# Kernel tuning notes

Hardware: AMD Instinct MI355X
Metric: run time of the kernel (lower is better)

Reference implementation:

```python
import jax, jax.numpy as jnp
import numpy as np

RADIUS = 1
WIN = 2 * RADIUS + 1


def setup_inputs() -> dict:
    key = jax.random.key(0)
    k1, k2 = jax.random.split(key)
    shape = (2, 64, 80, 80, 80)  # (b, c, d, h, w)
    x = jax.random.normal(k1, shape, dtype=jnp.float32)
    y = jax.random.normal(k2, shape, dtype=jnp.float32)
    return {"x": x, "y": y}


def reference(x, y):
    b, c, d, h, w = x.shape
    # zero-pad y by RADIUS on all three spatial dims
    y_padded = jnp.pad(
        y, ((0, 0), (0, 0), (RADIUS, RADIUS), (RADIUS, RADIUS), (RADIUS, RADIUS))
    )
    corrs = []
    for dz in range(WIN):
        for dy in range(WIN):
            for dx in range(WIN):
                y_win = y_padded[:, :, dz:dz + d, dy:dy + h, dx:dx + w]
                # channel-summed correlation for this offset -> [b, d, h, w]
                corrs.append(jnp.sum(x * y_win, axis=1))
    corr = jnp.stack(corrs, axis=1)
    return corr * (c ** -0.5)
```

## Files before the change

### kernel.cpp

```cpp
#include <hip/hip_runtime.h>

#define NT 320
#define TZ 4
#define TH 4
#define PZ 6
#define PH 6
#define STR 88
#define PROWS (PZ*PH)
#define NSLOT (PROWS*20)

__global__ __launch_bounds__(NT)
void wincorr_kernel(const float* __restrict__ x, const float* __restrict__ y,
                    float* __restrict__ out)
{
    __shared__ __align__(16) float buf[2][PROWS * STR];

    const long long plane = 512000;
    const int tid = threadIdx.x;
    const int twi = tid % 20;
    const int th  = (tid / 20) % TH;
    const int tz  = tid / 80;

    const int zt = blockIdx.x, ht = blockIdx.y, b = blockIdx.z;
    const int z0 = zt * TZ, h0 = ht * TH;
    const int gz = z0 + tz, gh = h0 + th, wb = 4 * twi;

    const float* xb = x + (long long)b * 64 * plane;
    const float* yb = y + (long long)b * 64 * plane;
    const long long xoff = (long long)gz * 6400 + gh * 80 + wb;

    int  goff[3], loff[3];
    bool val[3];
    const bool inr2 = (tid + 2 * NT) < NSLOT;
#pragma unroll
    for (int k = 0; k < 3; ++k) {
        int s   = tid + k * NT;
        int row = s / 20, col = s % 20;
        int pz = row / PH, py = row % PH;
        int yz = z0 - 1 + pz, yh = h0 - 1 + py;
        bool ok = (s < NSLOT) && ((unsigned)yz < 80u) && ((unsigned)yh < 80u);
        val[k]  = ok;
        goff[k] = yz * 6400 + yh * 80 + 4 * col;
        loff[k] = row * STR + 4 + 4 * col;
    }

    if (tid < 2 * PROWS) {
        int r = tid >> 1;
        int cix = (tid & 1) ? 84 : 3;
        buf[0][r * STR + cix] = 0.f;
        buf[1][r * STR + cix] = 0.f;
    }

    float4 acc[27];
#pragma unroll
    for (int o = 0; o < 27; ++o) acc[o] = make_float4(0.f, 0.f, 0.f, 0.f);

    const float4 zero4 = make_float4(0.f, 0.f, 0.f, 0.f);
    float4 v0, v1, v2;

    {
        const float* yc = yb;
        v0 = val[0] ? *(const float4*)(yc + goff[0]) : zero4;
        v1 = val[1] ? *(const float4*)(yc + goff[1]) : zero4;
        v2 = val[2] ? *(const float4*)(yc + goff[2]) : zero4;
        *(float4*)(&buf[0][loff[0]]) = v0;
        *(float4*)(&buf[0][loff[1]]) = v1;
        if (inr2) *(float4*)(&buf[0][loff[2]]) = v2;
    }
    __syncthreads();

    for (int c = 0; c < 64; ++c) {
        const float4 xv = *(const float4*)(xb + (long long)c * plane + xoff);

        if (c < 63) {
            const float* yc = yb + (long long)(c + 1) * plane;
            v0 = val[0] ? *(const float4*)(yc + goff[0]) : zero4;
            v1 = val[1] ? *(const float4*)(yc + goff[1]) : zero4;
            v2 = val[2] ? *(const float4*)(yc + goff[2]) : zero4;
        }

        const float* B = buf[c & 1];
#pragma unroll
        for (int dz = 0; dz < 3; ++dz) {
#pragma unroll
            for (int dy = 0; dy < 3; ++dy) {
                const float* rowp = B + ((tz + dz) * PH + (th + dy)) * STR + wb;
                const float4 r  = *(const float4*)(rowp + 4);
                const float rm1 = rowp[3];
                const float rp4 = rowp[8];
                const int o = (dz * 3 + dy) * 3;
                acc[o].x   += xv.x * rm1; acc[o].y   += xv.y * r.x;
                acc[o].z   += xv.z * r.y; acc[o].w   += xv.w * r.z;
                acc[o+1].x += xv.x * r.x; acc[o+1].y += xv.y * r.y;
                acc[o+1].z += xv.z * r.z; acc[o+1].w += xv.w * r.w;
                acc[o+2].x += xv.x * r.y; acc[o+2].y += xv.y * r.z;
                acc[o+2].z += xv.z * r.w; acc[o+2].w += xv.w * rp4;
            }
        }

        if (c < 63) {
            float* W = (float*)buf[(c + 1) & 1];
            *(float4*)(W + loff[0]) = v0;
            *(float4*)(W + loff[1]) = v1;
            if (inr2) *(float4*)(W + loff[2]) = v2;
        }
        __syncthreads();
    }

    float* ob = out + (long long)b * 27 * plane + xoff;
#pragma unroll
    for (int o = 0; o < 27; ++o) {
        float4 v = acc[o];
        v.x *= 0.125f; v.y *= 0.125f; v.z *= 0.125f; v.w *= 0.125f;
        *(float4*)(ob + (long long)o * plane) = v;
    }
}

extern "C" void kernel_launch(void* const* d_in, const int* in_sizes, int n_in,
                              void* d_out, int out_size, void* d_ws, size_t ws_size,
                              hipStream_t stream) {
    const float* x = (const float*)d_in[0];
    const float* y = (const float*)d_in[1];
    float* out = (float*)d_out;

    dim3 grid(80 / TZ, 80 / TH, 2);
    dim3 block(NT);
    wincorr_kernel<<<grid, block, 0, stream>>>(x, y, out);
}
```

Before: 750.6 us.

## Move the dx shift from shared-memory y reads onto x and output indexing

Instead of reading two extra unaligned scalars from shared memory per (dz,dy) row to form the dx=-1 and dx=+1 windows, each thread now reads only one aligned float4 of y. It loads two neighbouring x scalars from global memory per channel and writes the shifted results to output positions offset by one, zeroing the boundary columns explicitly. This cuts LDS reads in the inner loop and drops the padded halo columns, so the LDS row stride shrinks. In exchange it adds two scalar global loads per channel and turns the output stores into unaligned, partly scalar writes.

```diff
diff --git a/kernel.cpp b/kernel.cpp
--- a/kernel.cpp
+++ b/kernel.cpp
@@ -5,9 +5,13 @@
 #define TH 4
 #define PZ 6
 #define PH 6
-#define STR 88
+#define STR 84
 #define PROWS (PZ*PH)
 #define NSLOT (PROWS*20)
+
+__device__ __forceinline__ void store_f4u(float* p, float4 v) {
+    __builtin_memcpy(p, &v, 16);
+}
 
 __global__ __launch_bounds__(NT)
 void wincorr_kernel(const float* __restrict__ x, const float* __restrict__ y,
@@ -28,6 +32,8 @@
     const float* xb = x + (long long)b * 64 * plane;
     const float* yb = y + (long long)b * 64 * plane;
     const long long xoff = (long long)gz * 6400 + gh * 80 + wb;
+    const long long xoffm = xoff - (wb > 0 ? 1 : 0);
+    const long long xoffp = xoff + (wb < 76 ? 4 : 3);
 
     int  goff[3], loff[3];
     bool val[3];
@@ -41,14 +47,7 @@
         bool ok = (s < NSLOT) && ((unsigned)yz < 80u) && ((unsigned)yh < 80u);
         val[k]  = ok;
         goff[k] = yz * 6400 + yh * 80 + 4 * col;
-        loff[k] = row * STR + 4 + 4 * col;
-    }
-
-    if (tid < 2 * PROWS) {
-        int r = tid >> 1;
-        int cix = (tid & 1) ? 84 : 3;
-        buf[0][r * STR + cix] = 0.f;
-        buf[1][r * STR + cix] = 0.f;
+        loff[k] = row * STR + 4 * col;
     }
 
     float4 acc[27];
@@ -70,7 +69,10 @@
     __syncthreads();
 
     for (int c = 0; c < 64; ++c) {
-        const float4 xv = *(const float4*)(xb + (long long)c * plane + xoff);
+        const float* xcp = xb + (long long)c * plane;
+        const float4 xv  = *(const float4*)(xcp + xoff);
+        const float  xml = xcp[xoffm];
+        const float  xpr = xcp[xoffp];
 
         if (c < 63) {
             const float* yc = yb + (long long)(c + 1) * plane;
@@ -84,17 +86,14 @@
         for (int dz = 0; dz < 3; ++dz) {
 #pragma unroll
             for (int dy = 0; dy < 3; ++dy) {
-                const float* rowp = B + ((tz + dz) * PH + (th + dy)) * STR + wb;
-                const float4 r  = *(const float4*)(rowp + 4);
-                const float rm1 = rowp[3];
-                const float rp4 = rowp[8];
+                const float4 r = *(const float4*)(B + ((tz + dz) * PH + (th + dy)) * STR + wb);
                 const int o = (dz * 3 + dy) * 3;
-                acc[o].x   += xv.x * rm1; acc[o].y   += xv.y * r.x;
-                acc[o].z   += xv.z * r.y; acc[o].w   += xv.w * r.z;
+                acc[o].x   += xv.y * r.x; acc[o].y   += xv.z * r.y;
+                acc[o].z   += xv.w * r.z; acc[o].w   += xpr  * r.w;
                 acc[o+1].x += xv.x * r.x; acc[o+1].y += xv.y * r.y;
                 acc[o+1].z += xv.z * r.z; acc[o+1].w += xv.w * r.w;
-                acc[o+2].x += xv.x * r.y; acc[o+2].y += xv.y * r.z;
-                acc[o+2].z += xv.z * r.w; acc[o+2].w += xv.w * rp4;
+                acc[o+2].x += xml  * r.x; acc[o+2].y += xv.x * r.y;
+                acc[o+2].z += xv.y * r.z; acc[o+2].w += xv.z * r.w;
             }
         }
 
@@ -109,10 +108,25 @@
 
     float* ob = out + (long long)b * 27 * plane + xoff;
 #pragma unroll
-    for (int o = 0; o < 27; ++o) {
-        float4 v = acc[o];
-        v.x *= 0.125f; v.y *= 0.125f; v.z *= 0.125f; v.w *= 0.125f;
-        *(float4*)(ob + (long long)o * plane) = v;
+    for (int dz = 0; dz < 3; ++dz) {
+#pragma unroll
+        for (int dy = 0; dy < 3; ++dy) {
+            const int o = (dz * 3 + dy) * 3;
+            float4 a0 = acc[o], a1 = acc[o+1], a2 = acc[o+2];
+            a0.x *= 0.125f; a0.y *= 0.125f; a0.z *= 0.125f; a0.w *= 0.125f;
+            a1.x *= 0.125f; a1.y *= 0.125f; a1.z *= 0.125f; a1.w *= 0.125f;
+            a2.x *= 0.125f; a2.y *= 0.125f; a2.z *= 0.125f; a2.w *= 0.125f;
+            float* p0 = ob + (long long)(o    ) * plane;
+            float* p1 = ob + (long long)(o + 1) * plane;
+            float* p2 = ob + (long long)(o + 2) * plane;
+            if (twi < 19) store_f4u(p0 + 1, a0);
+            else { p0[1] = a0.x; p0[2] = a0.y; p0[3] = a0.z; }
+            if (twi == 0) p0[0] = 0.f;
+            *(float4*)p1 = a1;
+            if (twi > 0) store_f4u(p2 - 1, a2);
+            else { p2[0] = a2.y; p2[1] = a2.z; p2[2] = a2.w; }
+            if (twi == 19) p2[3] = 0.f;
+        }
     }
 }
 
```

After: 709.6 us. 1.06x faster.
